# Performance work log

Hardware: AMD Instinct MI355X
Metric: run time of the kernel (lower is better)

The kernel has to match this reference:

```python
import jax, jax.numpy as jnp
import numpy as np

B, T, C, H, DH = 2, 2048, 768, 12, 64


def setup_inputs() -> dict:
    key = jax.random.key(0)
    k1, k2, k3 = jax.random.split(key, 3)
    x = jax.random.normal(k1, (B, T, C), dtype=jnp.float32)
    Wqkv = jax.random.normal(k2, (C, 3 * C), dtype=jnp.float32) * (C ** -0.5)
    Wout = jax.random.normal(k3, (C, C), dtype=jnp.float32) * (C ** -0.5)
    return {"x": x, "Wqkv": Wqkv, "Wout": Wout}


def reference(x, Wqkv, Wout):
    b, t, c = x.shape
    qkv = x @ Wqkv  # [B,T,3C]
    q, k, v = jnp.split(qkv, 3, axis=-1)
    # [B,T,C] -> [B,H,T,dh]
    q = q.reshape(b, t, H, DH).transpose(0, 2, 1, 3)
    k = k.reshape(b, t, H, DH).transpose(0, 2, 1, 3)
    v = v.reshape(b, t, H, DH).transpose(0, 2, 1, 3)
    scale = DH ** -0.5
    scores = jnp.einsum('bhqd,bhkd->bhqk', q, k) * scale  # [B,H,T,T]
    causal = jnp.tril(jnp.ones((t, t), dtype=bool))
    scores = jnp.where(causal, scores, -jnp.inf)
    weights = jax.nn.softmax(scores, axis=-1)
    # dropout p=0.0 -> identity
    out = jnp.einsum('bhqk,bhkd->bhqd', weights, v)  # [B,H,T,dh]
    out = out.transpose(0, 2, 1, 3).reshape(b, t, c)
    return out @ Wout
```

## Files before the change

kernel.cpp:

```cpp
#include <hip/hip_runtime.h>
#include <hip/hip_bf16.h>

#define Bn 2
#define Tn 2048
#define Cn 768
#define Hn 12
#define Dn 64
#define N3n 2304
#define Mn 4096

#define MASKVAL (-30000.f)
#define NIT_G 144
#define DEFER_THR 64.f
#define L2E8 0.1803368801111204f

typedef unsigned short u16;
typedef __attribute__((ext_vector_type(8))) unsigned short ushort8_t;
typedef __attribute__((ext_vector_type(8))) short bf16x8;
typedef __attribute__((ext_vector_type(4))) float f32x4;
typedef __attribute__((ext_vector_type(2))) unsigned int uint2v;
typedef __attribute__((address_space(1))) unsigned int* gas1_t;
typedef __attribute__((address_space(3))) unsigned int* las3_t;

__device__ __forceinline__ float bf2f(u16 u) {
  union { unsigned int i; float f; } v; v.i = ((unsigned int)u) << 16; return v.f;
}
__device__ __forceinline__ u16 f2bf(float f) {
  union { float f; unsigned int i; } v; v.f = f;
  return (u16)((v.i + 0x7fffu + ((v.i >> 16) & 1u)) >> 16);
}

#define E(qt, s0, s1, ck) (((qt) << 24) | ((s0) << 16) | ((s1) << 8) | (ck))
__constant__ unsigned int SCHED[48] = {
    E(31, 0, 16, 0), E(31, 16, 32, 1), E(30, 0, 16, 0), E(15, 0, 16, 2),
    E(30, 16, 31, 1), E(29, 0, 15, 0), E(29, 15, 30, 1), E(28, 0, 15, 0), E(14, 0, 15, 2),
    E(28, 15, 29, 1), E(27, 0, 14, 0), E(27, 14, 28, 1), E(26, 0, 14, 0), E(13, 0, 14, 2),
    E(26, 14, 27, 1), E(25, 0, 13, 0), E(25, 13, 26, 1), E(24, 0, 13, 0), E(12, 0, 13, 2),
    E(24, 13, 25, 1), E(23, 0, 12, 0), E(23, 12, 24, 1), E(22, 0, 12, 0), E(11, 0, 12, 2),
    E(22, 12, 23, 1), E(21, 0, 11, 0), E(21, 11, 22, 1), E(20, 0, 11, 0), E(10, 0, 11, 2),
    E(20, 11, 21, 1), E(19, 0, 10, 0), E(19, 10, 20, 1), E(18, 0, 10, 0), E(9, 0, 10, 2),
    E(18, 10, 19, 1), E(17, 0, 9, 0), E(17, 9, 18, 1), E(16, 0, 9, 0), E(8, 0, 9, 2),
    E(16, 9, 17, 1), E(7, 0, 8, 2),
    E(6, 0, 7, 2), E(5, 0, 6, 2), E(4, 0, 5, 2), E(3, 0, 4, 2), E(2, 0, 3, 2),
    E(1, 0, 2, 2), E(0, 0, 1, 2)};

__global__ __launch_bounds__(256) void prep_kernel(const float* __restrict__ x,
                                                   const float* __restrict__ Wqkv,
                                                   const float* __restrict__ Wout,
                                                   u16* __restrict__ xb,
                                                   u16* __restrict__ WqkvT,
                                                   u16* __restrict__ WoutT,
                                                   int* __restrict__ counter) {
  __shared__ u16 t[32][33];
  const int bx = blockIdx.x;
  const int tid = threadIdx.x;
  if (bx < 3072) {
    if (bx == 0 && tid < 8) counter[tid] = 0;
    const int i = (bx * 256 + tid) * 4;
    float4 v = *(const float4*)(x + i);
    ushort4 s;
    s.x = f2bf(v.x); s.y = f2bf(v.y); s.z = f2bf(v.z); s.w = f2bf(v.w);
    *(ushort4*)(xb + i) = s;
  } else {
    const int idx = bx - 3072;
    const int gx = idx % 96, gy = idx / 96;
    const bool isA = gx < (N3n / 32);
    const float* in = isA ? Wqkv : Wout;
    u16* out = isA ? WqkvT : WoutT;
    const int Cc = isA ? N3n : Cn;
    const int c0 = (isA ? gx : gx - N3n / 32) * 32;
    const int r0 = gy * 32;
    const int tx = tid & 31, ty = tid >> 5;
#pragma unroll
    for (int i = 0; i < 4; i++)
      t[ty * 4 + i][tx] = f2bf(in[(size_t)(r0 + ty * 4 + i) * Cc + c0 + tx]);
    __syncthreads();
#pragma unroll
    for (int i = 0; i < 4; i++)
      out[(size_t)(c0 + ty * 4 + i) * Cn + r0 + tx] = t[tx][ty * 4 + i];
  }
}

#define BK 64

template <int EPI>
__global__ __launch_bounds__(256) void mfma_gemm(const u16* __restrict__ A,
                                                 const u16* __restrict__ BT,
                                                 u16* __restrict__ Q,
                                                 u16* __restrict__ Kd,
                                                 u16* __restrict__ VT,
                                                 float* __restrict__ out) {
  __shared__ __align__(16) u16 Ash[128 * BK];
  __shared__ __align__(16) u16 Bsh[128 * BK];
  const int tid = threadIdx.x;
  const int wv = tid >> 6, lane = tid & 63;
  const int lo = lane & 15, quad = lane >> 4;
  const int wm = wv & 1, wn = wv >> 1;

  const int nwg = gridDim.x * gridDim.y;
  const int cpx = nwg >> 3;
  const int lid = blockIdx.y * gridDim.x + blockIdx.x;
  const int swz = (lid & 7) * cpx + (lid >> 3);
  const int n0 = (swz % gridDim.x) * 128;
  const int m0 = (swz / gridDim.x) * 128;

  const int srow = lane >> 3;
  const int scol = (lane & 7) << 3;

  f32x4 acc[4][4];
#pragma unroll
  for (int i = 0; i < 4; i++)
#pragma unroll
    for (int j = 0; j < 4; j++) acc[i][j] = f32x4{0.f, 0.f, 0.f, 0.f};

  for (int k0 = 0; k0 < Cn; k0 += BK) {
    __syncthreads();
#pragma unroll
    for (int c = 0; c < 4; c++) {
      const int rb = (wv << 5) + (c << 3);
      const int gr = rb + srow;
      __builtin_amdgcn_global_load_lds(
          (gas1_t)(A + (size_t)(m0 + gr) * Cn + k0 + scol),
          (las3_t)(&Ash[rb * BK]), 16, 0, 0);
      __builtin_amdgcn_global_load_lds(
          (gas1_t)(BT + (size_t)(n0 + gr) * Cn + k0 + scol),
          (las3_t)(&Bsh[rb * BK]), 16, 0, 0);
    }
    __syncthreads();

    bf16x8 af[4][2], bfr[4][2];
#pragma unroll
    for (int t = 0; t < 4; t++) {
#pragma unroll
      for (int s = 0; s < 2; s++) {
        af[t][s]  = *(const bf16x8*)&Ash[(wm * 64 + t * 16 + lo) * BK + s * 32 + (quad << 3)];
        bfr[t][s] = *(const bf16x8*)&Bsh[(wn * 64 + t * 16 + lo) * BK + s * 32 + (quad << 3)];
      }
    }
#pragma unroll
    for (int mt = 0; mt < 4; mt++)
#pragma unroll
      for (int nt = 0; nt < 4; nt++) {
        acc[mt][nt] = __builtin_amdgcn_mfma_f32_16x16x32_bf16(af[mt][0], bfr[nt][0],
                                                              acc[mt][nt], 0, 0, 0);
        acc[mt][nt] = __builtin_amdgcn_mfma_f32_16x16x32_bf16(af[mt][1], bfr[nt][1],
                                                              acc[mt][nt], 0, 0, 0);
      }
  }

  if (EPI == 0) {
    const int which = n0 / Cn;
    const int h = ((n0 % Cn) >> 6) + wn;
    const int bb = m0 >> 11;
    const int t_base = (m0 & (Tn - 1)) + wm * 64;
    if (which < 2) {
      u16* dst = ((which == 0) ? Q : Kd) + (size_t)(bb * Hn + h) * Tn * Dn;
#pragma unroll
      for (int mt = 0; mt < 4; mt++)
#pragma unroll
        for (int nt = 0; nt < 4; nt++)
#pragma unroll
          for (int r = 0; r < 4; r++) {
            const int t = t_base + mt * 16 + (quad << 2) + r;
            dst[(size_t)t * Dn + nt * 16 + lo] = f2bf(acc[mt][nt][r]);
          }
    } else {
      u16* dst = VT + (size_t)(bb * Hn + h) * Dn * Tn;
#pragma unroll
      for (int mt = 0; mt < 4; mt++)
#pragma unroll
        for (int nt = 0; nt < 4; nt++) {
          const int t = t_base + mt * 16 + (quad << 2);
          const int d = nt * 16 + lo;
          ushort4 st;
          st.x = f2bf(acc[mt][nt][0]); st.y = f2bf(acc[mt][nt][1]);
          st.z = f2bf(acc[mt][nt][2]); st.w = f2bf(acc[mt][nt][3]);
          *(ushort4*)&dst[(size_t)d * Tn + t] = st;
        }
    }
  } else {
#pragma unroll
    for (int mt = 0; mt < 4; mt++)
#pragma unroll
      for (int nt = 0; nt < 4; nt++)
#pragma unroll
        for (int r = 0; r < 4; r++) {
          const int m = m0 + wm * 64 + mt * 16 + (quad << 2) + r;
          out[(size_t)m * Cn + n0 + wn * 64 + nt * 16 + lo] = acc[mt][nt][r];
        }
  }
}

#define TILE_W (64 * 64)

__global__ __launch_bounds__(256) void attn_kernel(const u16* __restrict__ Q,
                                                   const u16* __restrict__ K,
                                                   const u16* __restrict__ VT,
                                                   u16* __restrict__ O,
                                                   int* __restrict__ counter,
                                                   float* __restrict__ po,
                                                   float* __restrict__ pm,
                                                   float* __restrict__ pl) {
  __shared__ __align__(16) u16 Ksh[2 * TILE_W];
  __shared__ __align__(16) u16 Vsh[2 * TILE_W];
  int* sip = (int*)&Ksh[TILE_W];

  const int tid = threadIdx.x;
  const int g = blockIdx.x & 7;
  const int wv = tid >> 6, lane = tid & 63;
  const int lo = lane & 15, quad = lane >> 4;
  const int lo7 = lo & 7;
  const int ck0 = (quad ^ lo7) << 3;
  const int ck1 = ck0 ^ 32;
  const int sr = tid >> 3;
  const int sc = (tid & 7) << 3;
  const int kcol = ((lane & 7) ^ (lane >> 3)) << 3;
  const int t7 = tid & 7;
  const int vb0 = (((t7 & 6) ^ (sr & 7)) << 3) + ((t7 & 1) << 2);
  const int vb1 = ((((t7 & 6) | 1) ^ (sr & 7)) << 3) + ((t7 & 1) << 2);

  for (;;) {
    if (tid == 0) *sip = atomicAdd(&counter[g], 1);
    __syncthreads();
    const int il = *sip;
    if (il >= NIT_G) return;

    const unsigned int e = SCHED[il / 3];
    const int qt = e >> 24, ck = e & 255;
    const int jstart = ((e >> 16) & 255) << 6;
    const int jend   = ((e >> 8) & 255) << 6;
    const int q0 = qt << 6;
    const int hb = g * 3 + il % 3;
    const int h = hb % 12, b = hb / 12;
    const size_t base = (size_t)(b * Hn + h) * Tn * Dn;
    const size_t vtb  = (size_t)(b * Hn + h) * Dn * Tn;
    const u16* Kg = K + base;

    const u16* qp = Q + base + (size_t)(q0 + (wv << 4) + lo) * Dn + (quad << 3);
    const bf16x8 aq0 = *(const bf16x8*)qp;
    const bf16x8 aq1 = *(const bf16x8*)(qp + 32);

    f32x4 o[4] = {f32x4{0,0,0,0}, f32x4{0,0,0,0}, f32x4{0,0,0,0}, f32x4{0,0,0,0}};
    float m1 = MASKVAL;
    float l1 = 0.f;

#pragma unroll
    for (int c = 0; c < 2; c++) {
      const int rb = (wv << 4) + (c << 3);
      __builtin_amdgcn_global_load_lds(
          (gas1_t)(Kg + (size_t)(jstart + rb + (lane >> 3)) * Dn + kcol),
          (las3_t)(&Ksh[rb * 64]), 16, 0, 0);
    }
#pragma unroll
    for (int it = 0; it < 2; it++) {
      const int r = sr + it * 32;
      union { ushort8_t u; uint2v hh[2]; } vv;
      vv.u = *(const ushort8_t*)(VT + vtb + (size_t)r * Tn + jstart + sc);
      *(uint2v*)&Vsh[r * 64 + vb0] = vv.hh[0];
      *(uint2v*)&Vsh[r * 64 + vb1] = vv.hh[1];
    }
    __syncthreads();

    int cur = 0;
    const int qrel = (wv << 4) + lo;

    for (int j0 = jstart; j0 < jend; j0 += 64) {
      const bool hasnext = (j0 + 64 < jend);

      ushort8_t vr[2];
      if (hasnext) {
        const int nb = cur ^ 1;
#pragma unroll
        for (int c = 0; c < 2; c++) {
          const int rb = (wv << 4) + (c << 3);
          __builtin_amdgcn_global_load_lds(
              (gas1_t)(Kg + (size_t)(j0 + 64 + rb + (lane >> 3)) * Dn + kcol),
              (las3_t)(&Ksh[nb * TILE_W + rb * 64]), 16, 0, 0);
        }
#pragma unroll
        for (int it = 0; it < 2; it++) {
          const int r = sr + it * 32;
          vr[it] = *(const ushort8_t*)(VT + vtb + (size_t)r * Tn + j0 + 64 + sc);
        }
      }

      const u16* Kb_ = &Ksh[cur * TILE_W];
      const u16* Vb_ = &Vsh[cur * TILE_W];

      f32x4 s[4];
#pragma unroll
      for (int nt = 0; nt < 4; nt++) {
        const bf16x8 bk0 = *(const bf16x8*)(&Kb_[(nt * 16 + lo) * 64 + ck0]);
        const bf16x8 bk1 = *(const bf16x8*)(&Kb_[(nt * 16 + lo) * 64 + ck1]);
        f32x4 a = {0.f, 0.f, 0.f, 0.f};
        a = __builtin_amdgcn_mfma_f32_16x16x32_bf16(bk0, aq0, a, 0, 0, 0);
        a = __builtin_amdgcn_mfma_f32_16x16x32_bf16(bk1, aq1, a, 0, 0, 0);
        s[nt] = a;
      }

      if (j0 == q0) {
#pragma unroll
        for (int nt = 0; nt < 4; nt++)
#pragma unroll
          for (int r = 0; r < 4; r++) {
            const int kv = nt * 16 + (quad << 2) + r;
            if (kv > qrel) s[nt][r] = MASKVAL;
          }
      }

      const float mxa = fmaxf(fmaxf(s[0][0], s[0][1]), fmaxf(s[0][2], s[0][3]));
      const float mxb = fmaxf(fmaxf(s[1][0], s[1][1]), fmaxf(s[1][2], s[1][3]));
      const float mxc = fmaxf(fmaxf(s[2][0], s[2][1]), fmaxf(s[2][2], s[2][3]));
      const float mxd = fmaxf(fmaxf(s[3][0], s[3][1]), fmaxf(s[3][2], s[3][3]));
      const float pmax = fmaxf(fmaxf(mxa, mxb), fmaxf(mxc, mxd));

      if (!__all(pmax <= m1 + DEFER_THR)) {
        float mr = fmaxf(pmax, __shfl_xor(pmax, 16));
        mr = fmaxf(mr, __shfl_xor(mr, 32));
        const float mnew = fmaxf(m1, mr);
        const float alpha = __builtin_amdgcn_exp2f(L2E8 * (m1 - mnew));
        m1 = mnew;
        l1 *= alpha;
        float ar[4];
#pragma unroll
        for (int r = 0; r < 4; r++) ar[r] = __shfl(alpha, (quad << 2) + r);
#pragma unroll
        for (int nt = 0; nt < 4; nt++)
#pragma unroll
          for (int r = 0; r < 4; r++) o[nt][r] *= ar[r];
      }

      const float mb2 = L2E8 * m1;
#pragma unroll
      for (int nt = 0; nt < 4; nt++)
#pragma unroll
        for (int r = 0; r < 4; r++)
          s[nt][r] = __builtin_amdgcn_exp2f(L2E8 * s[nt][r] - mb2);
      {
        const float s0 = (s[0][0] + s[0][1]) + (s[0][2] + s[0][3]);
        const float s1 = (s[1][0] + s[1][1]) + (s[1][2] + s[1][3]);
        const float s2 = (s[2][0] + s[2][1]) + (s[2][2] + s[2][3]);
        const float s3 = (s[3][0] + s[3][1]) + (s[3][2] + s[3][3]);
        l1 += (s0 + s1) + (s2 + s3);
      }

      unsigned int A0, B0, A1, B1, A2, B2, A3, B3;
      asm("v_cvt_pk_bf16_f32 %0, %1, %2" : "=v"(A0) : "v"(s[0][0]), "v"(s[0][1]));
      asm("v_cvt_pk_bf16_f32 %0, %1, %2" : "=v"(B0) : "v"(s[0][2]), "v"(s[0][3]));
      asm("v_cvt_pk_bf16_f32 %0, %1, %2" : "=v"(A1) : "v"(s[1][0]), "v"(s[1][1]));
      asm("v_cvt_pk_bf16_f32 %0, %1, %2" : "=v"(B1) : "v"(s[1][2]), "v"(s[1][3]));
      asm("v_cvt_pk_bf16_f32 %0, %1, %2" : "=v"(A2) : "v"(s[2][0]), "v"(s[2][1]));
      asm("v_cvt_pk_bf16_f32 %0, %1, %2" : "=v"(B2) : "v"(s[2][2]), "v"(s[2][3]));
      asm("v_cvt_pk_bf16_f32 %0, %1, %2" : "=v"(A3) : "v"(s[3][0]), "v"(s[3][1]));
      asm("v_cvt_pk_bf16_f32 %0, %1, %2" : "=v"(B3) : "v"(s[3][2]), "v"(s[3][3]));
      const auto rA01 = __builtin_amdgcn_permlane32_swap(A0, A1, false, false);
      const auto rB01 = __builtin_amdgcn_permlane32_swap(B0, B1, false, false);
      const auto rA23 = __builtin_amdgcn_permlane32_swap(A2, A3, false, false);
      const auto rB23 = __builtin_amdgcn_permlane32_swap(B2, B3, false, false);
      union { unsigned int w[4]; bf16x8 v; } pa0u, pa1u;
      pa0u.w[0] = rA01[0]; pa0u.w[1] = rB01[0];
      pa0u.w[2] = rA01[1]; pa0u.w[3] = rB01[1];
      pa1u.w[0] = rA23[0]; pa1u.w[1] = rB23[0];
      pa1u.w[2] = rA23[1]; pa1u.w[3] = rB23[1];

#pragma unroll
      for (int nt = 0; nt < 4; nt++) {
        const bf16x8 bv0 = *(const bf16x8*)(&Vb_[(nt * 16 + lo) * 64 + ck0]);
        const bf16x8 bv1 = *(const bf16x8*)(&Vb_[(nt * 16 + lo) * 64 + ck1]);
        o[nt] = __builtin_amdgcn_mfma_f32_16x16x32_bf16(pa0u.v, bv0, o[nt], 0, 0, 0);
        o[nt] = __builtin_amdgcn_mfma_f32_16x16x32_bf16(pa1u.v, bv1, o[nt], 0, 0, 0);
      }

      if (hasnext) {
        const int nb = cur ^ 1;
#pragma unroll
        for (int it = 0; it < 2; it++) {
          const int r = sr + it * 32;
          union { ushort8_t u; uint2v hh[2]; } vv;
          vv.u = vr[it];
          *(uint2v*)&Vsh[nb * TILE_W + r * 64 + vb0] = vv.hh[0];
          *(uint2v*)&Vsh[nb * TILE_W + r * 64 + vb1] = vv.hh[1];
        }
      }
      __syncthreads();
      cur ^= 1;
    }

    float lt = l1;
    lt += __shfl_xor(lt, 16);
    lt += __shfl_xor(lt, 32);
    const float linv = 1.f / lt;
    float ir[4];
#pragma unroll
    for (int r = 0; r < 4; r++) ir[r] = __shfl(linv, (quad << 2) + r);

    if (ck == 2) {
#pragma unroll
      for (int nt = 0; nt < 4; nt++)
#pragma unroll
        for (int r = 0; r < 4; r++) {
          const int row = q0 + (wv << 4) + (quad << 2) + r;
          const int col = h * 64 + nt * 16 + lo;
          O[(size_t)(b * Tn + row) * Cn + col] = f2bf(o[nt][r] * ir[r]);
        }
    } else {
      const int st = hb * 16 + (qt - 16);
      const int pidx = st * 2 + ck;
      float* pO = po + ((size_t)pidx << 12);
#pragma unroll
      for (int nt = 0; nt < 4; nt++)
#pragma unroll
        for (int r = 0; r < 4; r++)
          pO[((wv << 4) + (quad << 2) + r) * 64 + nt * 16 + lo] = o[nt][r] * ir[r];
      if (quad == 0) {
        pm[pidx * 64 + (wv << 4) + lo] = m1;
        pl[pidx * 64 + (wv << 4) + lo] = lt;
      }
    }
  }
}

__global__ __launch_bounds__(256) void combine_kernel(const float* __restrict__ po,
                                                      const float* __restrict__ pm,
                                                      const float* __restrict__ pl,
                                                      u16* __restrict__ O) {
  const int st = blockIdx.x;
  const int hb = st >> 4;
  const int h = hb % 12, b = hb / 12;
  const int q0 = (16 + (st & 15)) << 6;
  const int tid = threadIdx.x;
  const int row = tid >> 2, cc0 = (tid & 3) << 4;
  const float* pa = po + (((size_t)st * 2) << 12) + row * 64 + cc0;
  const float* pb = pa + 4096;
  const float ma = pm[st * 128 + row],      la = pl[st * 128 + row];
  const float mb = pm[st * 128 + 64 + row], lb = pl[st * 128 + 64 + row];
  const float mm = fmaxf(ma, mb);
  float wa = la * __builtin_amdgcn_exp2f(L2E8 * (ma - mm));
  float wb = lb * __builtin_amdgcn_exp2f(L2E8 * (mb - mm));
  const float wi = 1.f / (wa + wb);
  wa *= wi; wb *= wi;
  u16* Orow = O + (size_t)(b * Tn + q0 + row) * Cn + h * 64 + cc0;
#pragma unroll
  for (int i = 0; i < 16; i += 4) {
    const float4 va = *(const float4*)(pa + i);
    const float4 vb = *(const float4*)(pb + i);
    ushort4 s4;
    s4.x = f2bf(wa * va.x + wb * vb.x);
    s4.y = f2bf(wa * va.y + wb * vb.y);
    s4.z = f2bf(wa * va.z + wb * vb.z);
    s4.w = f2bf(wa * va.w + wb * vb.w);
    *(ushort4*)(Orow + i) = s4;
  }
}

extern "C" void kernel_launch(void* const* d_in, const int* in_sizes, int n_in,
                              void* d_out, int out_size, void* d_ws, size_t ws_size,
                              hipStream_t stream) {
  const float* x    = (const float*)d_in[0];
  const float* Wqkv = (const float*)d_in[1];
  const float* Wout = (const float*)d_in[2];
  float* out = (float*)d_out;

  const size_t per = (size_t)Bn * Hn * Tn * Dn;
  u16* xb    = (u16*)d_ws;
  u16* WqkvT = xb + (size_t)Mn * Cn;
  u16* WoutT = WqkvT + (size_t)N3n * Cn;
  u16* Qb    = WoutT + (size_t)Cn * Cn;
  u16* Kb    = Qb + per;
  u16* VTb   = Kb + per;
  u16* attn  = VTb + per;
  int* counter = (int*)(attn + (size_t)Mn * Cn);
  float* po = (float*)(counter + 512);
  float* pm = po + (size_t)768 * 4096;
  float* pl = pm + (size_t)768 * 64;

  prep_kernel<<<dim3(3072 + 2304), 256, 0, stream>>>(x, Wqkv, Wout, xb, WqkvT,
                                                     WoutT, counter);
  mfma_gemm<0><<<dim3(N3n / 128, Mn / 128), 256, 0, stream>>>(xb, WqkvT, Qb, Kb, VTb, nullptr);
  attn_kernel<<<dim3(1024), 256, 0, stream>>>(Qb, Kb, VTb, attn, counter, po, pm, pl);
  combine_kernel<<<dim3(384), 256, 0, stream>>>(po, pm, pl, attn);
  mfma_gemm<1><<<dim3(Cn / 128, Mn / 128), 256, 0, stream>>>(attn, WoutT, nullptr, nullptr, nullptr, out);
}
```

Before: 179.9 us.

## Widen attention KV tile to 128 keys and rebuild split schedule

The attention kernel now processes 128 keys per iteration instead of 64. K and V shared buffers are doubled, and V is split into two 64-wide halves so each step issues four PV MFMAs. The causal mask is applied per element using global indices on any tile that overlaps the diagonal, the work schedule is re-expressed in 128-key units with a new ordering, and the launch drops to 512 persistent blocks. The aim is to halve loop and barrier overhead per key and amortise the softmax bookkeeping, at the cost of more shared memory and registers, lower occupancy, and more masked waste on diagonal tiles.

```diff
diff --git a/kernel.cpp b/kernel.cpp
--- a/kernel.cpp
+++ b/kernel.cpp
@@ -32,17 +32,20 @@
 
 #define E(qt, s0, s1, ck) (((qt) << 24) | ((s0) << 16) | ((s1) << 8) | (ck))
 __constant__ unsigned int SCHED[48] = {
-    E(31, 0, 16, 0), E(31, 16, 32, 1), E(30, 0, 16, 0), E(15, 0, 16, 2),
-    E(30, 16, 31, 1), E(29, 0, 15, 0), E(29, 15, 30, 1), E(28, 0, 15, 0), E(14, 0, 15, 2),
-    E(28, 15, 29, 1), E(27, 0, 14, 0), E(27, 14, 28, 1), E(26, 0, 14, 0), E(13, 0, 14, 2),
-    E(26, 14, 27, 1), E(25, 0, 13, 0), E(25, 13, 26, 1), E(24, 0, 13, 0), E(12, 0, 13, 2),
-    E(24, 13, 25, 1), E(23, 0, 12, 0), E(23, 12, 24, 1), E(22, 0, 12, 0), E(11, 0, 12, 2),
-    E(22, 12, 23, 1), E(21, 0, 11, 0), E(21, 11, 22, 1), E(20, 0, 11, 0), E(10, 0, 11, 2),
-    E(20, 11, 21, 1), E(19, 0, 10, 0), E(19, 10, 20, 1), E(18, 0, 10, 0), E(9, 0, 10, 2),
-    E(18, 10, 19, 1), E(17, 0, 9, 0), E(17, 9, 18, 1), E(16, 0, 9, 0), E(8, 0, 9, 2),
-    E(16, 9, 17, 1), E(7, 0, 8, 2),
-    E(6, 0, 7, 2), E(5, 0, 6, 2), E(4, 0, 5, 2), E(3, 0, 4, 2), E(2, 0, 3, 2),
-    E(1, 0, 2, 2), E(0, 0, 1, 2)};
+    E(31, 0, 8, 0), E(31, 8, 16, 1), E(30, 0, 8, 0), E(30, 8, 16, 1),
+    E(29, 0, 8, 0), E(28, 0, 8, 0), E(15, 0, 8, 2), E(14, 0, 8, 2),
+    E(29, 8, 15, 1), E(28, 8, 15, 1), E(27, 0, 7, 0), E(27, 7, 14, 1),
+    E(26, 0, 7, 0), E(26, 7, 14, 1), E(25, 0, 7, 0), E(24, 0, 7, 0),
+    E(13, 0, 7, 2), E(12, 0, 7, 2),
+    E(25, 7, 13, 1), E(24, 7, 13, 1), E(23, 0, 6, 0), E(23, 6, 12, 1),
+    E(22, 0, 6, 0), E(22, 6, 12, 1), E(21, 0, 6, 0), E(20, 0, 6, 0),
+    E(11, 0, 6, 2), E(10, 0, 6, 2),
+    E(21, 6, 11, 1), E(20, 6, 11, 1), E(19, 0, 5, 0), E(19, 5, 10, 1),
+    E(18, 0, 5, 0), E(18, 5, 10, 1), E(17, 0, 5, 0), E(16, 0, 5, 0),
+    E(9, 0, 5, 2), E(8, 0, 5, 2),
+    E(17, 5, 9, 1), E(16, 5, 9, 1), E(7, 0, 4, 2), E(6, 0, 4, 2),
+    E(5, 0, 3, 2), E(4, 0, 3, 2), E(3, 0, 2, 2), E(2, 0, 2, 2),
+    E(1, 0, 1, 2), E(0, 0, 1, 2)};
 
 __global__ __launch_bounds__(256) void prep_kernel(const float* __restrict__ x,
                                                    const float* __restrict__ Wqkv,
@@ -191,7 +194,8 @@
   }
 }
 
-#define TILE_W (64 * 64)
+#define KT_W (128 * 64)
+#define VH_W (64 * 64)
 
 __global__ __launch_bounds__(256) void attn_kernel(const u16* __restrict__ Q,
                                                    const u16* __restrict__ K,
@@ -201,9 +205,9 @@
                                                    float* __restrict__ po,
                                                    float* __restrict__ pm,
                                                    float* __restrict__ pl) {
-  __shared__ __align__(16) u16 Ksh[2 * TILE_W];
-  __shared__ __align__(16) u16 Vsh[2 * TILE_W];
-  int* sip = (int*)&Ksh[TILE_W];
+  __shared__ __align__(16) u16 Ksh[2 * KT_W];
+  __shared__ __align__(16) u16 Vsh[4 * VH_W];
+  int* sip = (int*)&Ksh[KT_W];
 
   const int tid = threadIdx.x;
   const int g = blockIdx.x & 7;
@@ -227,8 +231,8 @@
 
     const unsigned int e = SCHED[il / 3];
     const int qt = e >> 24, ck = e & 255;
-    const int jstart = ((e >> 16) & 255) << 6;
-    const int jend   = ((e >> 8) & 255) << 6;
+    const int jstart = ((e >> 16) & 255) << 7;
+    const int jend   = ((e >> 8) & 255) << 7;
     const int q0 = qt << 6;
     const int hb = g * 3 + il % 3;
     const int h = hb % 12, b = hb / 12;
@@ -245,51 +249,57 @@
     float l1 = 0.f;
 
 #pragma unroll
-    for (int c = 0; c < 2; c++) {
-      const int rb = (wv << 4) + (c << 3);
+    for (int c = 0; c < 4; c++) {
+      const int rb = (wv << 5) + (c << 3);
       __builtin_amdgcn_global_load_lds(
           (gas1_t)(Kg + (size_t)(jstart + rb + (lane >> 3)) * Dn + kcol),
           (las3_t)(&Ksh[rb * 64]), 16, 0, 0);
     }
 #pragma unroll
-    for (int it = 0; it < 2; it++) {
-      const int r = sr + it * 32;
-      union { ushort8_t u; uint2v hh[2]; } vv;
-      vv.u = *(const ushort8_t*)(VT + vtb + (size_t)r * Tn + jstart + sc);
-      *(uint2v*)&Vsh[r * 64 + vb0] = vv.hh[0];
-      *(uint2v*)&Vsh[r * 64 + vb1] = vv.hh[1];
-    }
+    for (int hf = 0; hf < 2; hf++)
+#pragma unroll
+      for (int it = 0; it < 2; it++) {
+        const int r = sr + it * 32;
+        union { ushort8_t u; uint2v hh[2]; } vv;
+        vv.u = *(const ushort8_t*)(VT + vtb + (size_t)r * Tn + jstart + hf * 64 + sc);
+        *(uint2v*)&Vsh[hf * VH_W + r * 64 + vb0] = vv.hh[0];
+        *(uint2v*)&Vsh[hf * VH_W + r * 64 + vb1] = vv.hh[1];
+      }
     __syncthreads();
 
     int cur = 0;
-    const int qrel = (wv << 4) + lo;
-
-    for (int j0 = jstart; j0 < jend; j0 += 64) {
-      const bool hasnext = (j0 + 64 < jend);
-
-      ushort8_t vr[2];
+    const int qg = q0 + (wv << 4) + lo;
+
+    for (int j0 = jstart; j0 < jend; j0 += 128) {
+      const bool hasnext = (j0 + 128 < jend);
+
+      ushort8_t vr[4];
       if (hasnext) {
         const int nb = cur ^ 1;
 #pragma unroll
-        for (int c = 0; c < 2; c++) {
-          const int rb = (wv << 4) + (c << 3);
+        for (int c = 0; c < 4; c++) {
+          const int rb = (wv << 5) + (c << 3);
           __builtin_amdgcn_global_load_lds(
-              (gas1_t)(Kg + (size_t)(j0 + 64 + rb + (lane >> 3)) * Dn + kcol),
-              (las3_t)(&Ksh[nb * TILE_W + rb * 64]), 16, 0, 0);
+              (gas1_t)(Kg + (size_t)(j0 + 128 + rb + (lane >> 3)) * Dn + kcol),
+              (las3_t)(&Ksh[nb * KT_W + rb * 64]), 16, 0, 0);
         }
 #pragma unroll
-        for (int it = 0; it < 2; it++) {
-          const int r = sr + it * 32;
-          vr[it] = *(const ushort8_t*)(VT + vtb + (size_t)r * Tn + j0 + 64 + sc);
-        }
-      }
-
-      const u16* Kb_ = &Ksh[cur * TILE_W];
-      const u16* Vb_ = &Vsh[cur * TILE_W];
-
-      f32x4 s[4];
-#pragma unroll
-      for (int nt = 0; nt < 4; nt++) {
+        for (int hf = 0; hf < 2; hf++)
+#pragma unroll
+          for (int it = 0; it < 2; it++) {
+            const int r = sr + it * 32;
+            vr[hf * 2 + it] =
+                *(const ushort8_t*)(VT + vtb + (size_t)r * Tn + j0 + 128 + hf * 64 + sc);
+          }
+      }
+
+      const u16* Kb_ = &Ksh[cur * KT_W];
+      const u16* VbA = &Vsh[cur * 2 * VH_W];
+      const u16* VbB = VbA + VH_W;
+
+      f32x4 s[8];
+#pragma unroll
+      for (int nt = 0; nt < 8; nt++) {
         const bf16x8 bk0 = *(const bf16x8*)(&Kb_[(nt * 16 + lo) * 64 + ck0]);
         const bf16x8 bk1 = *(const bf16x8*)(&Kb_[(nt * 16 + lo) * 64 + ck1]);
         f32x4 a = {0.f, 0.f, 0.f, 0.f};
@@ -298,21 +308,22 @@
         s[nt] = a;
       }
 
-      if (j0 == q0) {
-#pragma unroll
-        for (int nt = 0; nt < 4; nt++)
+      if (j0 + 128 > q0) {
+#pragma unroll
+        for (int nt = 0; nt < 8; nt++)
 #pragma unroll
           for (int r = 0; r < 4; r++) {
-            const int kv = nt * 16 + (quad << 2) + r;
-            if (kv > qrel) s[nt][r] = MASKVAL;
+            const int kvg = j0 + nt * 16 + (quad << 2) + r;
+            if (kvg > qg) s[nt][r] = MASKVAL;
           }
       }
 
-      const float mxa = fmaxf(fmaxf(s[0][0], s[0][1]), fmaxf(s[0][2], s[0][3]));
-      const float mxb = fmaxf(fmaxf(s[1][0], s[1][1]), fmaxf(s[1][2], s[1][3]));
-      const float mxc = fmaxf(fmaxf(s[2][0], s[2][1]), fmaxf(s[2][2], s[2][3]));
-      const float mxd = fmaxf(fmaxf(s[3][0], s[3][1]), fmaxf(s[3][2], s[3][3]));
-      const float pmax = fmaxf(fmaxf(mxa, mxb), fmaxf(mxc, mxd));
+      float gm[8];
+#pragma unroll
+      for (int nt = 0; nt < 8; nt++)
+        gm[nt] = fmaxf(fmaxf(s[nt][0], s[nt][1]), fmaxf(s[nt][2], s[nt][3]));
+      const float pmax = fmaxf(fmaxf(fmaxf(gm[0], gm[1]), fmaxf(gm[2], gm[3])),
+                               fmaxf(fmaxf(gm[4], gm[5]), fmaxf(gm[6], gm[7])));
 
       if (!__all(pmax <= m1 + DEFER_THR)) {
         float mr = fmaxf(pmax, __shfl_xor(pmax, 16));
@@ -332,19 +343,21 @@
 
       const float mb2 = L2E8 * m1;
 #pragma unroll
-      for (int nt = 0; nt < 4; nt++)
+      for (int nt = 0; nt < 8; nt++)
 #pragma unroll
         for (int r = 0; r < 4; r++)
           s[nt][r] = __builtin_amdgcn_exp2f(L2E8 * s[nt][r] - mb2);
       {
-        const float s0 = (s[0][0] + s[0][1]) + (s[0][2] + s[0][3]);
-        const float s1 = (s[1][0] + s[1][1]) + (s[1][2] + s[1][3]);
-        const float s2 = (s[2][0] + s[2][1]) + (s[2][2] + s[2][3]);
-        const float s3 = (s[3][0] + s[3][1]) + (s[3][2] + s[3][3]);
-        l1 += (s0 + s1) + (s2 + s3);
+        float gs[8];
+#pragma unroll
+        for (int nt = 0; nt < 8; nt++)
+          gs[nt] = (s[nt][0] + s[nt][1]) + (s[nt][2] + s[nt][3]);
+        l1 += ((gs[0] + gs[1]) + (gs[2] + gs[3])) +
+              ((gs[4] + gs[5]) + (gs[6] + gs[7]));
       }
 
       unsigned int A0, B0, A1, B1, A2, B2, A3, B3;
+      union { unsigned int w[4]; bf16x8 v; } pa0u, pa1u, pa2u, pa3u;
       asm("v_cvt_pk_bf16_f32 %0, %1, %2" : "=v"(A0) : "v"(s[0][0]), "v"(s[0][1]));
       asm("v_cvt_pk_bf16_f32 %0, %1, %2" : "=v"(B0) : "v"(s[0][2]), "v"(s[0][3]));
       asm("v_cvt_pk_bf16_f32 %0, %1, %2" : "=v"(A1) : "v"(s[1][0]), "v"(s[1][1]));
@@ -353,34 +366,59 @@
       asm("v_cvt_pk_bf16_f32 %0, %1, %2" : "=v"(B2) : "v"(s[2][2]), "v"(s[2][3]));
       asm("v_cvt_pk_bf16_f32 %0, %1, %2" : "=v"(A3) : "v"(s[3][0]), "v"(s[3][1]));
       asm("v_cvt_pk_bf16_f32 %0, %1, %2" : "=v"(B3) : "v"(s[3][2]), "v"(s[3][3]));
-      const auto rA01 = __builtin_amdgcn_permlane32_swap(A0, A1, false, false);
-      const auto rB01 = __builtin_amdgcn_permlane32_swap(B0, B1, false, false);
-      const auto rA23 = __builtin_amdgcn_permlane32_swap(A2, A3, false, false);
-      const auto rB23 = __builtin_amdgcn_permlane32_swap(B2, B3, false, false);
-      union { unsigned int w[4]; bf16x8 v; } pa0u, pa1u;
-      pa0u.w[0] = rA01[0]; pa0u.w[1] = rB01[0];
-      pa0u.w[2] = rA01[1]; pa0u.w[3] = rB01[1];
-      pa1u.w[0] = rA23[0]; pa1u.w[1] = rB23[0];
-      pa1u.w[2] = rA23[1]; pa1u.w[3] = rB23[1];
+      {
+        const auto rA01 = __builtin_amdgcn_permlane32_swap(A0, A1, false, false);
+        const auto rB01 = __builtin_amdgcn_permlane32_swap(B0, B1, false, false);
+        const auto rA23 = __builtin_amdgcn_permlane32_swap(A2, A3, false, false);
+        const auto rB23 = __builtin_amdgcn_permlane32_swap(B2, B3, false, false);
+        pa0u.w[0] = rA01[0]; pa0u.w[1] = rB01[0];
+        pa0u.w[2] = rA01[1]; pa0u.w[3] = rB01[1];
+        pa1u.w[0] = rA23[0]; pa1u.w[1] = rB23[0];
+        pa1u.w[2] = rA23[1]; pa1u.w[3] = rB23[1];
+      }
+      asm("v_cvt_pk_bf16_f32 %0, %1, %2" : "=v"(A0) : "v"(s[4][0]), "v"(s[4][1]));
+      asm("v_cvt_pk_bf16_f32 %0, %1, %2" : "=v"(B0) : "v"(s[4][2]), "v"(s[4][3]));
+      asm("v_cvt_pk_bf16_f32 %0, %1, %2" : "=v"(A1) : "v"(s[5][0]), "v"(s[5][1]));
+      asm("v_cvt_pk_bf16_f32 %0, %1, %2" : "=v"(B1) : "v"(s[5][2]), "v"(s[5][3]));
+      asm("v_cvt_pk_bf16_f32 %0, %1, %2" : "=v"(A2) : "v"(s[6][0]), "v"(s[6][1]));
+      asm("v_cvt_pk_bf16_f32 %0, %1, %2" : "=v"(B2) : "v"(s[6][2]), "v"(s[6][3]));
+      asm("v_cvt_pk_bf16_f32 %0, %1, %2" : "=v"(A3) : "v"(s[7][0]), "v"(s[7][1]));
+      asm("v_cvt_pk_bf16_f32 %0, %1, %2" : "=v"(B3) : "v"(s[7][2]), "v"(s[7][3]));
+      {
+        const auto rA01 = __builtin_amdgcn_permlane32_swap(A0, A1, false, false);
+        const auto rB01 = __builtin_amdgcn_permlane32_swap(B0, B1, false, false);
+        const auto rA23 = __builtin_amdgcn_permlane32_swap(A2, A3, false, false);
+        const auto rB23 = __builtin_amdgcn_permlane32_swap(B2, B3, false, false);
+        pa2u.w[0] = rA01[0]; pa2u.w[1] = rB01[0];
+        pa2u.w[2] = rA01[1]; pa2u.w[3] = rB01[1];
+        pa3u.w[0] = rA23[0]; pa3u.w[1] = rB23[0];
+        pa3u.w[2] = rA23[1]; pa3u.w[3] = rB23[1];
+      }
 
 #pragma unroll
       for (int nt = 0; nt < 4; nt++) {
-        const bf16x8 bv0 = *(const bf16x8*)(&Vb_[(nt * 16 + lo) * 64 + ck0]);
-        const bf16x8 bv1 = *(const bf16x8*)(&Vb_[(nt * 16 + lo) * 64 + ck1]);
-        o[nt] = __builtin_amdgcn_mfma_f32_16x16x32_bf16(pa0u.v, bv0, o[nt], 0, 0, 0);
-        o[nt] = __builtin_amdgcn_mfma_f32_16x16x32_bf16(pa1u.v, bv1, o[nt], 0, 0, 0);
+        const bf16x8 bvA0 = *(const bf16x8*)(&VbA[(nt * 16 + lo) * 64 + ck0]);
+        const bf16x8 bvA1 = *(const bf16x8*)(&VbA[(nt * 16 + lo) * 64 + ck1]);
+        const bf16x8 bvB0 = *(const bf16x8*)(&VbB[(nt * 16 + lo) * 64 + ck0]);
+        const bf16x8 bvB1 = *(const bf16x8*)(&VbB[(nt * 16 + lo) * 64 + ck1]);
+        o[nt] = __builtin_amdgcn_mfma_f32_16x16x32_bf16(pa0u.v, bvA0, o[nt], 0, 0, 0);
+        o[nt] = __builtin_amdgcn_mfma_f32_16x16x32_bf16(pa1u.v, bvA1, o[nt], 0, 0, 0);
+        o[nt] = __builtin_amdgcn_mfma_f32_16x16x32_bf16(pa2u.v, bvB0, o[nt], 0, 0, 0);
+        o[nt] = __builtin_amdgcn_mfma_f32_16x16x32_bf16(pa3u.v, bvB1, o[nt], 0, 0, 0);
       }
 
       if (hasnext) {
         const int nb = cur ^ 1;
 #pragma unroll
-        for (int it = 0; it < 2; it++) {
-          const int r = sr + it * 32;
-          union { ushort8_t u; uint2v hh[2]; } vv;
-          vv.u = vr[it];
-          *(uint2v*)&Vsh[nb * TILE_W + r * 64 + vb0] = vv.hh[0];
-          *(uint2v*)&Vsh[nb * TILE_W + r * 64 + vb1] = vv.hh[1];
-        }
+        for (int hf = 0; hf < 2; hf++)
+#pragma unroll
+          for (int it = 0; it < 2; it++) {
+            const int r = sr + it * 32;
+            union { ushort8_t u; uint2v hh[2]; } vv;
+            vv.u = vr[hf * 2 + it];
+            *(uint2v*)&Vsh[nb * 2 * VH_W + hf * VH_W + r * 64 + vb0] = vv.hh[0];
+            *(uint2v*)&Vsh[nb * 2 * VH_W + hf * VH_W + r * 64 + vb1] = vv.hh[1];
+          }
       }
       __syncthreads();
       cur ^= 1;
@@ -477,7 +515,7 @@
   prep_kernel<<<dim3(3072 + 2304), 256, 0, stream>>>(x, Wqkv, Wout, xb, WqkvT,
                                                      WoutT, counter);
   mfma_gemm<0><<<dim3(N3n / 128, Mn / 128), 256, 0, stream>>>(xb, WqkvT, Qb, Kb, VTb, nullptr);
-  attn_kernel<<<dim3(1024), 256, 0, stream>>>(Qb, Kb, VTb, attn, counter, po, pm, pl);
+  attn_kernel<<<dim3(512), 256, 0, stream>>>(Qb, Kb, VTb, attn, counter, po, pm, pl);
   combine_kernel<<<dim3(384), 256, 0, stream>>>(po, pm, pl, attn);
   mfma_gemm<1><<<dim3(Cn / 128, Mn / 128), 256, 0, stream>>>(attn, WoutT, nullptr, nullptr, nullptr, out);
 }
```

New measurement: 176.1 us. -2.1%, faster.
